# Performance work log

Hardware: AMD Instinct MI355X
Metric: run time of the kernel (lower is better)

Reference implementation:

```python
import jax, jax.numpy as jnp
import numpy as np

EPS = 1e-12  # torch F.normalize eps


def _l2_normalize(x):
    # matches torch.nn.functional.normalize(x, p=2, dim=-1)
    n = jnp.sqrt(jnp.sum(x * x, axis=-1, keepdims=True))
    return x / jnp.maximum(n, EPS)


def setup_inputs() -> dict:
    key = jax.random.key(0)
    k1, k2 = jax.random.split(key)
    b, i, m, kdim = 4, 25, 128, 64
    query = jax.random.normal(k1, (b, i, m, kdim), dtype=jnp.float32)
    support = jax.random.normal(k2, (b, i, m, kdim), dtype=jnp.float32)
    return {"query": query, "support": support}


def reference(query, support):
    """RelationGenerator.forward with way='cosine', mask=False.

    query:   [b, i, m, k]
    support: [b, j, n, k]
    returns: [b, i, j, m, n] cosine similarity matrix
    """
    qn = _l2_normalize(query)
    sn = _l2_normalize(support)
    # per-batch einsum 'imk,jnk->ijmn', stacked over b
    return jnp.einsum("bimk,bjnk->bijmn", qn, sn)
```

## Files before the change

kernel.cpp:

```cpp
#include <hip/hip_runtime.h>

typedef unsigned short u16;
typedef __attribute__((ext_vector_type(8))) short short8;
typedef __attribute__((ext_vector_type(4))) float floatx4;

#define QPITCH 72

__device__ __forceinline__ u16 f2bf(float x) {
    unsigned u = __float_as_uint(x);
    u += 0x7fffu + ((u >> 16) & 1u);
    return (u16)(u >> 16);
}

__global__ __launch_bounds__(256)
void cosine_relation_kernel(const float* __restrict__ q,
                            const float* __restrict__ s,
                            float* __restrict__ out)
{
    __shared__ u16 smem[2 * 128 * QPITCH];
    __shared__ float rq[128];
    __shared__ float rs[128];
    u16* qt = smem;
    u16* st = smem + 128 * QPITCH;

    const int t   = threadIdx.x;
    const int blk = blockIdx.x;
    const int b   = blk / 625;
    const int rem = blk % 625;
    const int i   = rem / 25;
    const int j   = rem % 25;

    const float* qbase = q + (size_t)(b * 25 + i) * 8192;
    const float* sbase = s + (size_t)(b * 25 + j) * 8192;

    const int row  = t >> 1;
    const int half = t & 1;
    {
        const float* gp = qbase + row * 64 + half * 32;
        u16*         lp = qt + row * QPITCH + half * 32;
        float ss = 0.f;
#pragma unroll
        for (int c = 0; c < 4; ++c) {
            float4 f0 = *(const float4*)(gp + c * 8);
            float4 f1 = *(const float4*)(gp + c * 8 + 4);
            ss += f0.x*f0.x + f0.y*f0.y + f0.z*f0.z + f0.w*f0.w;
            ss += f1.x*f1.x + f1.y*f1.y + f1.z*f1.z + f1.w*f1.w;
            short8 h;
            h[0] = (short)f2bf(f0.x); h[1] = (short)f2bf(f0.y);
            h[2] = (short)f2bf(f0.z); h[3] = (short)f2bf(f0.w);
            h[4] = (short)f2bf(f1.x); h[5] = (short)f2bf(f1.y);
            h[6] = (short)f2bf(f1.z); h[7] = (short)f2bf(f1.w);
            *(short8*)(lp + c * 8) = h;
        }
        ss += __shfl_xor(ss, 1);
        if (half == 0) rq[row] = 1.0f / fmaxf(sqrtf(ss), 1e-12f);
    }
    {
        const float* gp = sbase + row * 64 + half * 32;
        u16*         lp = st + row * QPITCH + half * 32;
        float ss = 0.f;
#pragma unroll
        for (int c = 0; c < 4; ++c) {
            float4 f0 = *(const float4*)(gp + c * 8);
            float4 f1 = *(const float4*)(gp + c * 8 + 4);
            ss += f0.x*f0.x + f0.y*f0.y + f0.z*f0.z + f0.w*f0.w;
            ss += f1.x*f1.x + f1.y*f1.y + f1.z*f1.z + f1.w*f1.w;
            short8 h;
            h[0] = (short)f2bf(f0.x); h[1] = (short)f2bf(f0.y);
            h[2] = (short)f2bf(f0.z); h[3] = (short)f2bf(f0.w);
            h[4] = (short)f2bf(f1.x); h[5] = (short)f2bf(f1.y);
            h[6] = (short)f2bf(f1.z); h[7] = (short)f2bf(f1.w);
            *(short8*)(lp + c * 8) = h;
        }
        ss += __shfl_xor(ss, 1);
        if (half == 0) rs[row] = 1.0f / fmaxf(sqrtf(ss), 1e-12f);
    }
    __syncthreads();

    const int wave = t >> 6;
    const int lane = t & 63;
    const int quad = lane >> 4;
    const int l15  = lane & 15;
    const int m0   = (wave >> 1) * 64;
    const int n0   = (wave & 1) * 64;

    floatx4 acc[4][4] = {};
#pragma unroll
    for (int ks = 0; ks < 2; ++ks) {
        short8 af[4], bfr[4];
#pragma unroll
        for (int mt = 0; mt < 4; ++mt)
            af[mt] = *(const short8*)(qt + (m0 + mt * 16 + l15) * QPITCH + ks * 32 + quad * 8);
#pragma unroll
        for (int nt = 0; nt < 4; ++nt)
            bfr[nt] = *(const short8*)(st + (n0 + nt * 16 + l15) * QPITCH + ks * 32 + quad * 8);
#pragma unroll
        for (int mt = 0; mt < 4; ++mt)
#pragma unroll
            for (int nt = 0; nt < 4; ++nt)
                acc[mt][nt] = __builtin_amdgcn_mfma_f32_16x16x32_bf16(
                    af[mt], bfr[nt], acc[mt][nt], 0, 0, 0);
    }

    float rsv[4];
#pragma unroll
    for (int nt = 0; nt < 4; ++nt) rsv[nt] = rs[n0 + nt * 16 + l15];
    float rqv[4][4];
#pragma unroll
    for (int mt = 0; mt < 4; ++mt)
#pragma unroll
        for (int r = 0; r < 4; ++r) rqv[mt][r] = rq[m0 + mt * 16 + quad * 4 + r];

    float* obase = out + (size_t)blk * 16384 + n0 + l15;
#pragma unroll
    for (int mt = 0; mt < 4; ++mt) {
#pragma unroll
        for (int r = 0; r < 4; ++r) {
            const int m = m0 + mt * 16 + quad * 4 + r;
            float* op = obase + m * 128;
#pragma unroll
            for (int nt = 0; nt < 4; ++nt)
                op[nt * 16] = acc[mt][nt][r] * rqv[mt][r] * rsv[nt];
        }
    }
}

extern "C" void kernel_launch(void* const* d_in, const int* in_sizes, int n_in,
                              void* d_out, int out_size, void* d_ws, size_t ws_size,
                              hipStream_t stream) {
    const float* q = (const float*)d_in[0];
    const float* s = (const float*)d_in[1];
    float* out = (float*)d_out;
    cosine_relation_kernel<<<2500, 256, 0, stream>>>(q, s, out);
}
```

Measured before the change: 179.9 us.

## Pre-normalize rows before bf16 packing and drop epilogue scaling

```diff
diff --git a/kernel.cpp b/kernel.cpp
--- a/kernel.cpp
+++ b/kernel.cpp
@@ -1,25 +1,26 @@
 #include <hip/hip_runtime.h>
 
 typedef unsigned short u16;
+typedef unsigned int u32;
 typedef __attribute__((ext_vector_type(8))) short short8;
 typedef __attribute__((ext_vector_type(4))) float floatx4;
+typedef __attribute__((ext_vector_type(4))) u32 uint4v;
 
 #define QPITCH 72
 
-__device__ __forceinline__ u16 f2bf(float x) {
-    unsigned u = __float_as_uint(x);
-    u += 0x7fffu + ((u >> 16) & 1u);
-    return (u16)(u >> 16);
+__device__ __forceinline__ u32 pack2bf(float a, float b) {
+    u32 ua = __float_as_uint(a), ub = __float_as_uint(b);
+    ua += 0x7fffu + ((ua >> 16) & 1u);
+    ub += 0x7fffu + ((ub >> 16) & 1u);
+    return __builtin_amdgcn_perm(ub, ua, 0x07060302);
 }
 
-__global__ __launch_bounds__(256)
+__global__ __launch_bounds__(256, 4)
 void cosine_relation_kernel(const float* __restrict__ q,
                             const float* __restrict__ s,
                             float* __restrict__ out)
 {
     __shared__ u16 smem[2 * 128 * QPITCH];
-    __shared__ float rq[128];
-    __shared__ float rs[128];
     u16* qt = smem;
     u16* st = smem + 128 * QPITCH;
 
@@ -35,45 +36,28 @@
 
     const int row  = t >> 1;
     const int half = t & 1;
-    {
-        const float* gp = qbase + row * 64 + half * 32;
-        u16*         lp = qt + row * QPITCH + half * 32;
+#pragma unroll
+    for (int tile = 0; tile < 2; ++tile) {
+        const float* gp = (tile == 0 ? qbase : sbase) + row * 64 + half * 32;
+        u16*         lp = (tile == 0 ? qt : st) + row * QPITCH + half * 32;
+        float4 f[8];
+#pragma unroll
+        for (int c = 0; c < 8; ++c) f[c] = ((const float4*)gp)[c];
         float ss = 0.f;
 #pragma unroll
-        for (int c = 0; c < 4; ++c) {
-            float4 f0 = *(const float4*)(gp + c * 8);
-            float4 f1 = *(const float4*)(gp + c * 8 + 4);
-            ss += f0.x*f0.x + f0.y*f0.y + f0.z*f0.z + f0.w*f0.w;
-            ss += f1.x*f1.x + f1.y*f1.y + f1.z*f1.z + f1.w*f1.w;
-            short8 h;
-            h[0] = (short)f2bf(f0.x); h[1] = (short)f2bf(f0.y);
-            h[2] = (short)f2bf(f0.z); h[3] = (short)f2bf(f0.w);
-            h[4] = (short)f2bf(f1.x); h[5] = (short)f2bf(f1.y);
-            h[6] = (short)f2bf(f1.z); h[7] = (short)f2bf(f1.w);
-            *(short8*)(lp + c * 8) = h;
-        }
+        for (int c = 0; c < 8; ++c)
+            ss += f[c].x*f[c].x + f[c].y*f[c].y + f[c].z*f[c].z + f[c].w*f[c].w;
         ss += __shfl_xor(ss, 1);
-        if (half == 0) rq[row] = 1.0f / fmaxf(sqrtf(ss), 1e-12f);
-    }
-    {
-        const float* gp = sbase + row * 64 + half * 32;
-        u16*         lp = st + row * QPITCH + half * 32;
-        float ss = 0.f;
+        const float r = 1.0f / fmaxf(sqrtf(ss), 1e-12f);
 #pragma unroll
         for (int c = 0; c < 4; ++c) {
-            float4 f0 = *(const float4*)(gp + c * 8);
-            float4 f1 = *(const float4*)(gp + c * 8 + 4);
-            ss += f0.x*f0.x + f0.y*f0.y + f0.z*f0.z + f0.w*f0.w;
-            ss += f1.x*f1.x + f1.y*f1.y + f1.z*f1.z + f1.w*f1.w;
-            short8 h;
-            h[0] = (short)f2bf(f0.x); h[1] = (short)f2bf(f0.y);
-            h[2] = (short)f2bf(f0.z); h[3] = (short)f2bf(f0.w);
-            h[4] = (short)f2bf(f1.x); h[5] = (short)f2bf(f1.y);
-            h[6] = (short)f2bf(f1.z); h[7] = (short)f2bf(f1.w);
-            *(short8*)(lp + c * 8) = h;
+            uint4v pk;
+            pk.x = pack2bf(f[2*c].x * r,   f[2*c].y * r);
+            pk.y = pack2bf(f[2*c].z * r,   f[2*c].w * r);
+            pk.z = pack2bf(f[2*c+1].x * r, f[2*c+1].y * r);
+            pk.w = pack2bf(f[2*c+1].z * r, f[2*c+1].w * r);
+            *(uint4v*)(lp + c * 8) = pk;
         }
-        ss += __shfl_xor(ss, 1);
-        if (half == 0) rs[row] = 1.0f / fmaxf(sqrtf(ss), 1e-12f);
     }
     __syncthreads();
 
@@ -102,25 +86,15 @@
                     af[mt], bfr[nt], acc[mt][nt], 0, 0, 0);
     }
 
-    float rsv[4];
-#pragma unroll
-    for (int nt = 0; nt < 4; ++nt) rsv[nt] = rs[n0 + nt * 16 + l15];
-    float rqv[4][4];
-#pragma unroll
-    for (int mt = 0; mt < 4; ++mt)
-#pragma unroll
-        for (int r = 0; r < 4; ++r) rqv[mt][r] = rq[m0 + mt * 16 + quad * 4 + r];
-
     float* obase = out + (size_t)blk * 16384 + n0 + l15;
 #pragma unroll
     for (int mt = 0; mt < 4; ++mt) {
 #pragma unroll
         for (int r = 0; r < 4; ++r) {
-            const int m = m0 + mt * 16 + quad * 4 + r;
-            float* op = obase + m * 128;
+            float* op = obase + (size_t)(m0 + mt * 16 + quad * 4 + r) * 128;
 #pragma unroll
             for (int nt = 0; nt < 4; ++nt)
-                op[nt * 16] = acc[mt][nt][r] * rqv[mt][r] * rsv[nt];
+                op[nt * 16] = acc[mt][nt][r];
         }
     }
 }
```

Result: no change. 176.4 us (-1.9%).
